# Kernel optimization log

Hardware: AMD Instinct MI355X
Metric: run time of the kernel (lower is better)

## Reference

```python
import jax, jax.numpy as jnp
import numpy as np

DIM = 1024
HEADS = 16
HEAD_DIM = DIM // HEADS


def setup_inputs() -> dict:
    key = jax.random.key(0)
    k_x, k_qkv, k_ow, k_ob = jax.random.split(key, 4)
    x = jax.random.normal(k_x, (2, 2048, DIM), dtype=jnp.float32)
    # nn.Linear(dim, 3*dim, bias=False): weight shape [3*dim, dim], y = x @ W.T
    w_qkv = jax.random.normal(k_qkv, (3 * DIM, DIM), dtype=jnp.float32) * (DIM ** -0.5)
    # nn.Linear(dim, dim) with bias
    w_o = jax.random.normal(k_ow, (DIM, DIM), dtype=jnp.float32) * (DIM ** -0.5)
    b_o = jax.random.normal(k_ob, (DIM,), dtype=jnp.float32) * 0.02
    return {"x": x, "w_qkv": w_qkv, "w_o": w_o, "b_o": b_o}


def reference(x, w_qkv, w_o, b_o):
    b, n, _ = x.shape
    scale = DIM ** -0.5  # NOTE: source scales by full dim, not head dim
    # qkv projection: [b, n, 3*dim]
    qkv = jnp.einsum('bnd,ed->bne', x, w_qkv)
    # 'b n (qkv h d) -> qkv b h n d'
    qkv = qkv.reshape(b, n, 3, HEADS, HEAD_DIM)
    q = jnp.transpose(qkv[:, :, 0], (0, 2, 1, 3))  # [b, h, n, d]
    k = jnp.transpose(qkv[:, :, 1], (0, 2, 1, 3))
    v = jnp.transpose(qkv[:, :, 2], (0, 2, 1, 3))
    scores = jnp.einsum('bhqd,bhkd->bhqk', q, k) * scale  # [b, h, n, n]
    attn = jax.nn.softmax(scores, axis=-1)
    out = jnp.einsum('bhqk,bhkd->bhqd', attn, v)  # [b, h, n, d]
    out = jnp.transpose(out, (0, 2, 1, 3)).reshape(b, n, DIM)  # 'b h n d -> b n (h d)'
    out = jnp.einsum('bnd,ed->bne', out, w_o) + b_o
    return out
```

## Files before the change

### kernel.cpp

```cpp
#include <hip/hip_runtime.h>
#include <stdint.h>


#define DIM 1024
#define SEQ 2048
#define BATCH 2
#define ROWS 4096
#define RSTRIDE 3072

typedef __bf16 bf16_t;
typedef bf16_t bf16x4 __attribute__((ext_vector_type(4)));
typedef bf16_t bf16x8 __attribute__((ext_vector_type(8)));
typedef float f32x4 __attribute__((ext_vector_type(4)));
typedef short s16x4 __attribute__((ext_vector_type(4)));

__device__ __forceinline__ ushort f2bf(float f) {
    uint32_t u;
    __builtin_memcpy(&u, &f, 4);
    uint32_t r = (u + 0x7fffu + ((u >> 16) & 1u)) >> 16;
    return (ushort)r;
}

__device__ __forceinline__ void store_out(ushort* p, float v) { *p = f2bf(v); }
__device__ __forceinline__ void store_out(float* p, float v) { *p = v; }

__device__ __forceinline__ void gl_lds16(const void* g, void* l) {
    __builtin_amdgcn_global_load_lds(
        (const __attribute__((address_space(1))) void*)g,
        (__attribute__((address_space(3))) void*)l, 16, 0, 0);
}

__global__ __launch_bounds__(256) void cvt3_kernel(
    const float* __restrict__ x, const float* __restrict__ wq,
    const float* __restrict__ wo, ushort* __restrict__ dst) {
    size_t i = ((size_t)blockIdx.x * 256 + threadIdx.x) * 8;
    const size_t n_x = (size_t)ROWS * DIM;
    const size_t n_wq = (size_t)3 * DIM * DIM;
    const float* src;
    size_t off;
    if (i < n_x) {
        src = x; off = i;
    } else if (i < n_x + n_wq) {
        src = wq; off = i - n_x;
    } else {
        src = wo; off = i - n_x - n_wq;
    }
    float4 a = *(const float4*)(src + off);
    float4 b = *(const float4*)(src + off + 4);
    uint4 u;
    u.x = (uint)f2bf(a.x) | ((uint)f2bf(a.y) << 16);
    u.y = (uint)f2bf(a.z) | ((uint)f2bf(a.w) << 16);
    u.z = (uint)f2bf(b.x) | ((uint)f2bf(b.y) << 16);
    u.w = (uint)f2bf(b.z) | ((uint)f2bf(b.w) << 16);
    *(uint4*)(dst + i) = u;
}

template <typename OutT, int BN>
__global__ __launch_bounds__(256) void gemm_bt_kernel(
    const ushort* __restrict__ A, const ushort* __restrict__ B,
    const float* __restrict__ bias, OutT* __restrict__ C,
    int M, int N, int K) {
    constexpr int JN = BN / 32;
    __shared__ __align__(16) ushort sA[128 * 64];
    __shared__ __align__(16) ushort sB[BN * 64];

    const int tid = threadIdx.x;
    const int lane = tid & 63, w = tid >> 6;
    const int quad = lane >> 4, l15 = lane & 15;
    const int wm = (w >> 1) * 64, wn = (w & 1) * (BN / 2);
    const int bm = blockIdx.y, bn = blockIdx.x;

    f32x4 acc[4][JN];
#pragma unroll
    for (int i = 0; i < 4; i++)
#pragma unroll
        for (int j = 0; j < JN; j++) acc[i][j] = (f32x4){0.f, 0.f, 0.f, 0.f};

    const ushort* Abase = A + (size_t)(bm * 128) * K;
    const ushort* Bbase = B + (size_t)(bn * BN) * K;
    const int rd = lane >> 3, c8 = lane & 7;
    const int sw = l15 & 7;

    for (int kk = 0; kk < K; kk += 64) {
        __syncthreads();
#pragma unroll
        for (int t = 0; t < 4; t++) {
            int row = w * 32 + t * 8;
            gl_lds16(Abase + (size_t)(row + rd) * K + kk + ((c8 ^ rd) * 8),
                     sA + row * 64);
        }
#pragma unroll
        for (int t = 0; t < BN / 32; t++) {
            int row = w * 8 + t * 32;
            gl_lds16(Bbase + (size_t)(row + rd) * K + kk + ((c8 ^ rd) * 8),
                     sB + row * 64);
        }
        __syncthreads();

#pragma unroll
        for (int kh = 0; kh < 2; kh++) {
            bf16x8 af[4], bfr[JN];
#pragma unroll
            for (int i = 0; i < 4; i++)
                af[i] = *(const bf16x8*)((const bf16_t*)sA +
                        (wm + i * 16 + l15) * 64 + (((kh * 4 + quad) ^ sw) * 8));
#pragma unroll
            for (int j = 0; j < JN; j++)
                bfr[j] = *(const bf16x8*)((const bf16_t*)sB +
                        (wn + j * 16 + l15) * 64 + (((kh * 4 + quad) ^ sw) * 8));
#pragma unroll
            for (int i = 0; i < 4; i++)
#pragma unroll
                for (int j = 0; j < JN; j++)
                    acc[i][j] = __builtin_amdgcn_mfma_f32_16x16x32_bf16(
                        af[i], bfr[j], acc[i][j], 0, 0, 0);
        }
    }

#pragma unroll
    for (int i = 0; i < 4; i++)
#pragma unroll
        for (int j = 0; j < JN; j++) {
            int col = bn * BN + wn + j * 16 + l15;
            float bv = bias ? bias[col] : 0.f;
#pragma unroll
            for (int r = 0; r < 4; r++) {
                int row = bm * 128 + wm + i * 16 + quad * 4 + r;
                store_out(&C[(size_t)row * N + col], acc[i][j][r] + bv);
            }
        }
}

__global__ __launch_bounds__(512, 4) void flash_attn_kernel(
    const ushort* __restrict__ qkv, ushort* __restrict__ out) {
    __shared__ __align__(16) ushort sK[128 * 64];
    __shared__ __align__(16) ushort sVt[64 * 128];

    const int tid = threadIdx.x;
    const int lane = tid & 63, w = tid >> 6;
    const int quad = lane >> 4, l15 = lane & 15;
    const int sw = l15 & 7;
    const int qh = quad >> 1, q1 = quad & 1;
    const int bh = blockIdx.y, b = bh >> 4, h = bh & 15;
    const int q0 = blockIdx.x * 128;
    const ushort* qkvb = qkv + (size_t)b * SEQ * RSTRIDE + h * 64;

    const ushort* qrow = qkvb + (size_t)(q0 + w * 16 + l15) * RSTRIDE;
    const bf16x8 aq0 = *(const bf16x8*)(qrow + quad * 8);
    const bf16x8 aq1 = *(const bf16x8*)(qrow + 32 + quad * 8);

    const int krow = tid >> 3, kc8 = tid & 7;
    const int kdst = krow * 64 + ((kc8 ^ (krow & 7)) * 8);
    const int vrp = tid & 63, vc = tid >> 6;
    const int vch = vrp >> 2, vlo = vrp & 3;

    uint4 kreg0, kreg1, va, vb;
    {
        const ushort* kp0 = qkvb + (size_t)krow * RSTRIDE + DIM + kc8 * 8;
        kreg0 = *(const uint4*)kp0;
        kreg1 = *(const uint4*)(kp0 + (size_t)64 * RSTRIDE);
        const ushort* v0 = qkvb + (size_t)(2 * vrp) * RSTRIDE + 2 * DIM + vc * 8;
        va = *(const uint4*)v0;
        vb = *(const uint4*)(v0 + RSTRIDE);
    }

    f32x4 l_acc = (f32x4){0.f, 0.f, 0.f, 0.f};
    f32x4 o[4];
#pragma unroll
    for (int j = 0; j < 4; j++) o[j] = (f32x4){0.f, 0.f, 0.f, 0.f};

    s16x4 vones;
#pragma unroll
    for (int e = 0; e < 4; e++) vones[e] = (short)0x3F80;

    const float c_exp = 0.04508422f;

    uint* vt32 = (uint*)sVt;
    for (int kb = 0; kb < SEQ; kb += 128) {
        *(uint4*)(sK + kdst) = kreg0;
        *(uint4*)(sK + 64 * 64 + kdst) = kreg1;
        {
            int base = (vc * 8) * 64 + vlo;
            vt32[base + 0 * 64 + ((vch ^ 0) << 2)] = (va.x & 0xffffu) | (vb.x << 16);
            vt32[base + 1 * 64 + ((vch ^ 1) << 2)] = (va.x >> 16) | (vb.x & 0xffff0000u);
            vt32[base + 2 * 64 + ((vch ^ 2) << 2)] = (va.y & 0xffffu) | (vb.y << 16);
            vt32[base + 3 * 64 + ((vch ^ 3) << 2)] = (va.y >> 16) | (vb.y & 0xffff0000u);
            vt32[base + 4 * 64 + ((vch ^ 4) << 2)] = (va.z & 0xffffu) | (vb.z << 16);
            vt32[base + 5 * 64 + ((vch ^ 5) << 2)] = (va.z >> 16) | (vb.z & 0xffff0000u);
            vt32[base + 6 * 64 + ((vch ^ 6) << 2)] = (va.w & 0xffffu) | (vb.w << 16);
            vt32[base + 7 * 64 + ((vch ^ 7) << 2)] = (va.w >> 16) | (vb.w & 0xffff0000u);
        }
        __syncthreads();

        int nkb = (kb + 128 < SEQ) ? kb + 128 : kb;
        {
            const ushort* kp0 = qkvb + (size_t)(nkb + krow) * RSTRIDE + DIM + kc8 * 8;
            kreg0 = *(const uint4*)kp0;
            kreg1 = *(const uint4*)(kp0 + (size_t)64 * RSTRIDE);
            const ushort* v0 =
                qkvb + (size_t)(nkb + 2 * vrp) * RSTRIDE + 2 * DIM + vc * 8;
            va = *(const uint4*)v0;
            vb = *(const uint4*)(v0 + RSTRIDE);
        }

        f32x4 s[8];
#pragma unroll
        for (int j = 0; j < 8; j++) {
            const ushort* kp = sK + (j * 16 + l15) * 64;
            bf16x8 bk0 = *(const bf16x8*)(kp + ((quad ^ sw) * 8));
            bf16x8 bk1 = *(const bf16x8*)(kp + (((4 | quad) ^ sw) * 8));
            f32x4 z = (f32x4){0.f, 0.f, 0.f, 0.f};
            __builtin_amdgcn_s_setprio(1);
            z = __builtin_amdgcn_mfma_f32_16x16x32_bf16(bk0, aq0, z, 0, 0, 0);
            z = __builtin_amdgcn_mfma_f32_16x16x32_bf16(bk1, aq1, z, 0, 0, 0);
            __builtin_amdgcn_s_setprio(0);
            s[j] = z;
        }

        s16x4 pa[8];
#pragma unroll
        for (int j = 0; j < 8; j++) {
            bf16x4 t;
#pragma unroll
            for (int r = 0; r < 4; r++)
                t[r] = (bf16_t)__builtin_amdgcn_exp2f(s[j][r] * c_exp);
            pa[j] = __builtin_bit_cast(s16x4, t);
        }

        __builtin_amdgcn_s_setprio(1);
#pragma unroll
        for (int j = 0; j < 8; j++)
            l_acc = __builtin_amdgcn_mfma_f32_16x16x16bf16_1k(
                pa[j], vones, l_acc, 0, 0, 0);
        __builtin_amdgcn_s_setprio(0);

#pragma unroll
        for (int jd = 0; jd < 4; jd++) {
            const bf16_t* vp = (const bf16_t*)sVt + (jd * 16 + l15) * 128;
            __builtin_amdgcn_s_setprio(1);
#pragma unroll
            for (int j = 0; j < 8; j++) {
                int ch = 2 * j + qh;
                bf16x4 bv = *(const bf16x4*)(vp + ((ch ^ sw) * 8 + q1 * 4));
                o[jd] = __builtin_amdgcn_mfma_f32_16x16x16bf16_1k(
                    pa[j], __builtin_bit_cast(s16x4, bv), o[jd], 0, 0, 0);
            }
            __builtin_amdgcn_s_setprio(0);
        }
        __syncthreads();
    }

#pragma unroll
    for (int r = 0; r < 4; r++) {
        float inv = 1.f / l_acc[r];
        int qrow_i = q0 + w * 16 + quad * 4 + r;
#pragma unroll
        for (int j = 0; j < 4; j++) {
            out[(size_t)(b * SEQ + qrow_i) * DIM + h * 64 + j * 16 + l15] =
                f2bf(o[j][r] * inv);
        }
    }
}

extern "C" void kernel_launch(void* const* d_in, const int* in_sizes, int n_in,
                              void* d_out, int out_size, void* d_ws, size_t ws_size,
                              hipStream_t stream) {
    const float* x = (const float*)d_in[0];
    const float* w_qkv = (const float*)d_in[1];
    const float* w_o = (const float*)d_in[2];
    const float* b_o = (const float*)d_in[3];
    float* out = (float*)d_out;

    ushort* qkv = (ushort*)d_ws;
    ushort* attn = qkv + (size_t)ROWS * 3 * DIM;
    ushort* xb = attn + (size_t)ROWS * DIM;
    ushort* wqkvb = xb + (size_t)ROWS * DIM;
    ushort* wob = wqkvb + (size_t)3 * DIM * DIM;

    dim3 blk(256);
    cvt3_kernel<<<(ROWS * DIM + 3 * DIM * DIM + DIM * DIM) / 2048, blk, 0,
                  stream>>>(x, w_qkv, w_o, xb);

    gemm_bt_kernel<ushort, 128>
        <<<dim3(3 * DIM / 128, ROWS / 128), blk, 0, stream>>>(
            xb, wqkvb, nullptr, qkv, ROWS, 3 * DIM, DIM);
    flash_attn_kernel<<<dim3(SEQ / 128, BATCH * 16), dim3(512), 0, stream>>>(qkv, attn);
    gemm_bt_kernel<float, 64>
        <<<dim3(DIM / 64, ROWS / 128), blk, 0, stream>>>(
            attn, wob, b_o, out, ROWS, DIM, DIM);
}
```

Baseline: 187.6 us.

## Double-buffer K/V tiles in LDS for flash attention

Doubles the shared-memory K and V^T buffers so the next tile is written into the alternate buffer while the current one feeds the MFMAs. Global loads are issued two tiles ahead. The aim is to hide the store-then-barrier latency that previously stalled every iteration. LDS use doubles to 64KB per block, which could reduce occupancy relative to the launch bound of 4 blocks.

```diff
diff --git a/kernel.cpp b/kernel.cpp
--- a/kernel.cpp
+++ b/kernel.cpp
@@ -133,8 +133,8 @@
 
 __global__ __launch_bounds__(512, 4) void flash_attn_kernel(
     const ushort* __restrict__ qkv, ushort* __restrict__ out) {
-    __shared__ __align__(16) ushort sK[128 * 64];
-    __shared__ __align__(16) ushort sVt[64 * 128];
+    __shared__ __align__(16) ushort sK[2][128 * 64];
+    __shared__ __align__(16) ushort sVt[2][64 * 128];
 
     const int tid = threadIdx.x;
     const int lane = tid & 63, w = tid >> 6;
@@ -175,38 +175,47 @@
 
     const float c_exp = 0.04508422f;
 
-    uint* vt32 = (uint*)sVt;
+#define STAGE_KV(KBUF, VBUF32)                                                  \
+    do {                                                                        \
+        *(uint4*)((KBUF) + kdst) = kreg0;                                       \
+        *(uint4*)((KBUF) + 64 * 64 + kdst) = kreg1;                             \
+        int base = (vc * 8) * 64 + vlo;                                         \
+        (VBUF32)[base + 0 * 64 + ((vch ^ 0) << 2)] = (va.x & 0xffffu) | (vb.x << 16); \
+        (VBUF32)[base + 1 * 64 + ((vch ^ 1) << 2)] = (va.x >> 16) | (vb.x & 0xffff0000u); \
+        (VBUF32)[base + 2 * 64 + ((vch ^ 2) << 2)] = (va.y & 0xffffu) | (vb.y << 16); \
+        (VBUF32)[base + 3 * 64 + ((vch ^ 3) << 2)] = (va.y >> 16) | (vb.y & 0xffff0000u); \
+        (VBUF32)[base + 4 * 64 + ((vch ^ 4) << 2)] = (va.z & 0xffffu) | (vb.z << 16); \
+        (VBUF32)[base + 5 * 64 + ((vch ^ 5) << 2)] = (va.z >> 16) | (vb.z & 0xffff0000u); \
+        (VBUF32)[base + 6 * 64 + ((vch ^ 6) << 2)] = (va.w & 0xffffu) | (vb.w << 16); \
+        (VBUF32)[base + 7 * 64 + ((vch ^ 7) << 2)] = (va.w >> 16) | (vb.w & 0xffff0000u); \
+    } while (0)
+
+#define LOAD_KV(NKB)                                                            \
+    do {                                                                        \
+        const ushort* kp0 =                                                     \
+            qkvb + (size_t)((NKB) + krow) * RSTRIDE + DIM + kc8 * 8;            \
+        kreg0 = *(const uint4*)kp0;                                             \
+        kreg1 = *(const uint4*)(kp0 + (size_t)64 * RSTRIDE);                    \
+        const ushort* v0 =                                                      \
+            qkvb + (size_t)((NKB) + 2 * vrp) * RSTRIDE + 2 * DIM + vc * 8;      \
+        va = *(const uint4*)v0;                                                 \
+        vb = *(const uint4*)(v0 + RSTRIDE);                                     \
+    } while (0)
+
+    STAGE_KV(sK[0], (uint*)sVt[0]);
+    LOAD_KV(128);
+    __syncthreads();
+
     for (int kb = 0; kb < SEQ; kb += 128) {
-        *(uint4*)(sK + kdst) = kreg0;
-        *(uint4*)(sK + 64 * 64 + kdst) = kreg1;
-        {
-            int base = (vc * 8) * 64 + vlo;
-            vt32[base + 0 * 64 + ((vch ^ 0) << 2)] = (va.x & 0xffffu) | (vb.x << 16);
-            vt32[base + 1 * 64 + ((vch ^ 1) << 2)] = (va.x >> 16) | (vb.x & 0xffff0000u);
-            vt32[base + 2 * 64 + ((vch ^ 2) << 2)] = (va.y & 0xffffu) | (vb.y << 16);
-            vt32[base + 3 * 64 + ((vch ^ 3) << 2)] = (va.y >> 16) | (vb.y & 0xffff0000u);
-            vt32[base + 4 * 64 + ((vch ^ 4) << 2)] = (va.z & 0xffffu) | (vb.z << 16);
-            vt32[base + 5 * 64 + ((vch ^ 5) << 2)] = (va.z >> 16) | (vb.z & 0xffff0000u);
-            vt32[base + 6 * 64 + ((vch ^ 6) << 2)] = (va.w & 0xffffu) | (vb.w << 16);
-            vt32[base + 7 * 64 + ((vch ^ 7) << 2)] = (va.w >> 16) | (vb.w & 0xffff0000u);
-        }
-        __syncthreads();
-
-        int nkb = (kb + 128 < SEQ) ? kb + 128 : kb;
-        {
-            const ushort* kp0 = qkvb + (size_t)(nkb + krow) * RSTRIDE + DIM + kc8 * 8;
-            kreg0 = *(const uint4*)kp0;
-            kreg1 = *(const uint4*)(kp0 + (size_t)64 * RSTRIDE);
-            const ushort* v0 =
-                qkvb + (size_t)(nkb + 2 * vrp) * RSTRIDE + 2 * DIM + vc * 8;
-            va = *(const uint4*)v0;
-            vb = *(const uint4*)(v0 + RSTRIDE);
-        }
+        const int c = (kb >> 7) & 1;
+        STAGE_KV(sK[c ^ 1], (uint*)sVt[c ^ 1]);
+        int nkb = (kb + 256 < SEQ) ? kb + 256 : kb;
+        LOAD_KV(nkb);
 
         f32x4 s[8];
 #pragma unroll
         for (int j = 0; j < 8; j++) {
-            const ushort* kp = sK + (j * 16 + l15) * 64;
+            const ushort* kp = sK[c] + (j * 16 + l15) * 64;
             bf16x8 bk0 = *(const bf16x8*)(kp + ((quad ^ sw) * 8));
             bf16x8 bk1 = *(const bf16x8*)(kp + (((4 | quad) ^ sw) * 8));
             f32x4 z = (f32x4){0.f, 0.f, 0.f, 0.f};
@@ -236,7 +245,7 @@
 
 #pragma unroll
         for (int jd = 0; jd < 4; jd++) {
-            const bf16_t* vp = (const bf16_t*)sVt + (jd * 16 + l15) * 128;
+            const bf16_t* vp = (const bf16_t*)sVt[c] + (jd * 16 + l15) * 128;
             __builtin_amdgcn_s_setprio(1);
 #pragma unroll
             for (int j = 0; j < 8; j++) {
@@ -260,6 +269,8 @@
                 f2bf(o[j][r] * inv);
         }
     }
+#undef STAGE_KV
+#undef LOAD_KV
 }
 
 extern "C" void kernel_launch(void* const* d_in, const int* in_sizes, int n_in,
```

Result: no change. 191.1 us (+1.9%).
